# Kernel tuning notes

Hardware: AMD Instinct MI355X
Metric: run time of the kernel (lower is better)

Reference implementation:

```python
import jax, jax.numpy as jnp
import numpy as np

H, DH = 8, 64            # heads, dim_head (module defaults)
B, N, DN, DE = 1, 512, 128, 64  # batch, nodes, node feat, edge feat
INNER = H * DH


def _w(key, fan_in, fan_out):
    return jax.random.normal(key, (fan_in, fan_out), jnp.float32) / np.sqrt(fan_in)


def setup_inputs() -> dict:
    key = jax.random.key(0)
    ks = jax.random.split(key, 8)
    return {
        "nodes": jax.random.normal(ks[0], (B, N, DN), jnp.float32),
        "edges": jax.random.normal(ks[1], (B, N, N, DE), jnp.float32),
        "mask": jnp.ones((B, N), dtype=bool),
        "Wq": _w(ks[2], DN, INNER), "bq": jnp.zeros((INNER,), jnp.float32),
        "Wk": _w(ks[3], DN, INNER), "bk": jnp.zeros((INNER,), jnp.float32),
        "Wv": _w(ks[4], DN, INNER), "bv": jnp.zeros((INNER,), jnp.float32),
        "We": _w(ks[5], DE, INNER), "be": jnp.zeros((INNER,), jnp.float32),
        "Wo": _w(ks[6], INNER, DN), "bo": jnp.zeros((DN,), jnp.float32),
    }


def _split_heads(x):
    # (b, ..., h*d) -> (b*h, ..., d), matching rearrange 'b ... (h d) -> (b h) ... d'
    b = x.shape[0]
    mid = x.shape[1:-1]
    x = x.reshape(b, *mid, H, DH)
    x = jnp.moveaxis(x, -2, 1)              # (b, h, ..., d)
    return x.reshape(b * H, *mid, DH)


def reference(nodes, edges, mask, Wq, bq, Wk, bk, Wv, bv, We, be, Wo, bo):
    scale = DH ** (-0.5)
    q = _split_heads(nodes @ Wq + bq)        # (bh, n, d)
    k = _split_heads(nodes @ Wk + bk)        # (bh, n, d)
    v = _split_heads(nodes @ Wv + bv)        # (bh, n, d)
    e = _split_heads(edges @ We + be)        # (bh, n, n, d) -- ek == ev == e_kv
    k = k[:, None, :, :] + e                 # (bh, i, j, d) per-ij keys
    v = v[:, None, :, :] + e                 # (bh, i, j, d) per-ij values
    sim = jnp.einsum('bid,bijd->bij', q, k) * scale
    m = mask[:, :, None] & mask[:, None, :]  # (b, i, j)
    m = jnp.repeat(m, H, axis=0)             # (bh, i, j)
    sim = jnp.where(m, sim, -jnp.finfo(sim.dtype).max)
    attn = jax.nn.softmax(sim, axis=-1)
    out = jnp.einsum('bij,bijd->bid', attn, v)           # (bh, n, d)
    out = out.reshape(B, H, N, DH).transpose(0, 2, 1, 3).reshape(B, N, INNER)
    return out @ Wo + bo                                  # (b, n, d_node)
```

## Files before the change

### kernel.cpp

```cpp
#include <hip/hip_runtime.h>
#include <hip/hip_bf16.h>

#define NN 512
#define DNODE 128
#define DEDGE 64
#define NH 8
#define DHD 64
#define DIN 512
#define SCALE 0.125f

typedef unsigned short u16;
typedef unsigned int u32;

__device__ __forceinline__ float bf2f(u16 b) {
    u32 u = ((u32)b) << 16;
    return __builtin_bit_cast(float, u);
}
__device__ __forceinline__ u16 f2bf(float f) {
    u32 u = __builtin_bit_cast(u32, f);
    return (u16)((u + 0x7fffu + ((u >> 16) & 1u)) >> 16);
}
__device__ __forceinline__ float bflo(u32 u) { return __builtin_bit_cast(float, u << 16); }
__device__ __forceinline__ float bfhi(u32 u) { return __builtin_bit_cast(float, u & 0xffff0000u); }

__global__ __launch_bounds__(256) void k_qkv(
    const float* __restrict__ nodes,
    const float* __restrict__ Wq, const float* __restrict__ bq,
    const float* __restrict__ Wk, const float* __restrict__ bk,
    const float* __restrict__ Wv, const float* __restrict__ bv,
    float* __restrict__ Qo, float* __restrict__ Ko, float* __restrict__ Vo)
{
    const int it = blockIdx.x, ct = blockIdx.y, which = blockIdx.z;
    const float* W    = which == 0 ? Wq : (which == 1 ? Wk : Wv);
    const float* bias = which == 0 ? bq : (which == 1 ? bk : bv);
    float* O          = which == 0 ? Qo : (which == 1 ? Ko : Vo);
    __shared__ float As[64][132];
    __shared__ float Bs[128][68];
    const int t = threadIdx.x;
    const int ibase = it * 64, cbase = ct * 64;
#pragma unroll
    for (int p = 0; p < 8; ++p) {
        int r = p * 8 + (t >> 5), c4 = (t & 31) * 4;
        *(float4*)&As[r][c4] = *(const float4*)(nodes + (ibase + r) * DNODE + c4);
    }
#pragma unroll
    for (int p = 0; p < 8; ++p) {
        int k = p * 16 + (t >> 4), c4 = (t & 15) * 4;
        *(float4*)&Bs[k][c4] = *(const float4*)(W + k * DIN + cbase + c4);
    }
    __syncthreads();
    const int tx = t & 15, ty = t >> 4;
    float acc[4][4] = {};
    for (int k = 0; k < DNODE; ++k) {
        float4 b4 = *(const float4*)&Bs[k][tx * 4];
#pragma unroll
        for (int e = 0; e < 4; ++e) {
            float a = As[ty * 4 + e][k];
            acc[e][0] += a * b4.x; acc[e][1] += a * b4.y;
            acc[e][2] += a * b4.z; acc[e][3] += a * b4.w;
        }
    }
    const int h = ct;
#pragma unroll
    for (int ii = 0; ii < 4; ++ii) {
        int i = ibase + ty * 4 + ii;
        float4 o;
        o.x = acc[ii][0] + bias[cbase + tx * 4 + 0];
        o.y = acc[ii][1] + bias[cbase + tx * 4 + 1];
        o.z = acc[ii][2] + bias[cbase + tx * 4 + 2];
        o.w = acc[ii][3] + bias[cbase + tx * 4 + 3];
        *(float4*)(O + ((size_t)h * NN + i) * DHD + tx * 4) = o;
    }
}

__global__ __launch_bounds__(256) void k_qe(
    const float* __restrict__ Q, const float* __restrict__ We, float* __restrict__ QE)
{
    const int it = blockIdx.x, h = blockIdx.y;
    __shared__ float Qs[64][68];
    __shared__ float WsT[64][68];
    const int t = threadIdx.x;
    const int ibase = it * 64;
#pragma unroll
    for (int p = 0; p < 4; ++p) {
        int r = p * 16 + (t >> 4), d4 = (t & 15) * 4;
        *(float4*)&Qs[r][d4] = *(const float4*)(Q + ((size_t)h * NN + ibase + r) * DHD + d4);
    }
#pragma unroll
    for (int p = 0; p < 4; ++p) {
        int c = p * 16 + (t >> 4), d4 = (t & 15) * 4;
        float4 v = *(const float4*)(We + c * DIN + h * DHD + d4);
        WsT[d4 + 0][c] = v.x; WsT[d4 + 1][c] = v.y;
        WsT[d4 + 2][c] = v.z; WsT[d4 + 3][c] = v.w;
    }
    __syncthreads();
    const int tx = t & 15, ty = t >> 4;
    float acc[4][4] = {};
    for (int d = 0; d < DHD; ++d) {
        float4 b4 = *(const float4*)&WsT[d][tx * 4];
#pragma unroll
        for (int e = 0; e < 4; ++e) {
            float a = Qs[ty * 4 + e][d];
            acc[e][0] += a * b4.x; acc[e][1] += a * b4.y;
            acc[e][2] += a * b4.z; acc[e][3] += a * b4.w;
        }
    }
#pragma unroll
    for (int ii = 0; ii < 4; ++ii) {
        int i = ibase + ty * 4 + ii;
        float4 o;
        o.x = SCALE * acc[ii][0]; o.y = SCALE * acc[ii][1];
        o.z = SCALE * acc[ii][2]; o.w = SCALE * acc[ii][3];
        *(float4*)(QE + ((size_t)h * NN + i) * DEDGE + tx * 4) = o;
    }
}

__global__ __launch_bounds__(256) void k_qk(
    const float* __restrict__ Q, const float* __restrict__ K, float* __restrict__ QK)
{
    const int jt = blockIdx.x, it = blockIdx.y, h = blockIdx.z;
    __shared__ float Qs[64][68];
    __shared__ float KsT[64][68];
    const int t = threadIdx.x;
    const int ibase = it * 64, jbase = jt * 64;
#pragma unroll
    for (int p = 0; p < 4; ++p) {
        int r = p * 16 + (t >> 4), d4 = (t & 15) * 4;
        *(float4*)&Qs[r][d4] = *(const float4*)(Q + ((size_t)h * NN + ibase + r) * DHD + d4);
    }
#pragma unroll
    for (int p = 0; p < 4; ++p) {
        int j = p * 16 + (t >> 4), d4 = (t & 15) * 4;
        float4 v = *(const float4*)(K + ((size_t)h * NN + jbase + j) * DHD + d4);
        KsT[d4 + 0][j] = v.x; KsT[d4 + 1][j] = v.y;
        KsT[d4 + 2][j] = v.z; KsT[d4 + 3][j] = v.w;
    }
    __syncthreads();
    const int tx = t & 15, ty = t >> 4;
    float acc[4][4] = {};
    for (int d = 0; d < DHD; ++d) {
        float4 b4 = *(const float4*)&KsT[d][tx * 4];
#pragma unroll
        for (int e = 0; e < 4; ++e) {
            float a = Qs[ty * 4 + e][d];
            acc[e][0] += a * b4.x; acc[e][1] += a * b4.y;
            acc[e][2] += a * b4.z; acc[e][3] += a * b4.w;
        }
    }
#pragma unroll
    for (int ii = 0; ii < 4; ++ii) {
        int i = ibase + ty * 4 + ii;
        float4 o;
        o.x = SCALE * acc[ii][0]; o.y = SCALE * acc[ii][1];
        o.z = SCALE * acc[ii][2]; o.w = SCALE * acc[ii][3];
        *(float4*)(QK + ((size_t)h * NN + i) * NN + jbase + tx * 4) = o;
    }
}

__global__ __launch_bounds__(512, 4) void k_fused(
    const float* __restrict__ edges, const float* __restrict__ QK,
    const float* __restrict__ QE, float* __restrict__ AE, u16* __restrict__ P)
{
    __shared__ u16 erow[NN * 64];
    __shared__ u16 PlT[NH * 520];
    __shared__ float qes[NH][DEDGE];
    __shared__ float ae_acc[NH * 65];
    const int i = blockIdx.x;
    const int t = threadIdx.x;
    const int lane = t & 63, w = t >> 6;

    const float* E = edges + (size_t)i * NN * DEDGE;
    const int jst = t >> 3, c0 = (t & 7) * 8;
    float4 fa[8], fb[8];
#pragma unroll
    for (int p = 0; p < 8; ++p) {
        const float* s = E + (p * 64 + jst) * 64 + c0;
        fa[p] = *(const float4*)s;
        fb[p] = *(const float4*)(s + 4);
    }
    const float* qk = QK + ((size_t)w * NN + i) * NN;
    float qkr[8];
#pragma unroll
    for (int r = 0; r < 8; ++r) qkr[r] = qk[r * 64 + lane];
    qes[w][lane] = QE[((size_t)w * NN + i) * DEDGE + lane];
#pragma unroll
    for (int z = t; z < NH * 65; z += 512) ae_acc[z] = 0.f;

#pragma unroll
    for (int p = 0; p < 8; ++p) {
        int j = p * 64 + jst;
        uint4 pk;
        pk.x = (u32)f2bf(fa[p].x) | ((u32)f2bf(fa[p].y) << 16);
        pk.y = (u32)f2bf(fa[p].z) | ((u32)f2bf(fa[p].w) << 16);
        pk.z = (u32)f2bf(fb[p].x) | ((u32)f2bf(fb[p].y) << 16);
        pk.w = (u32)f2bf(fb[p].z) | ((u32)f2bf(fb[p].w) << 16);
        int sb = (j * 128 + c0 * 2) ^ ((j & 7) << 4);
        *(uint4*)((char*)erow + sb) = pk;
    }
    __syncthreads();

    float sim[8];
#pragma unroll
    for (int r = 0; r < 8; ++r) sim[r] = qkr[r];
#pragma unroll
    for (int cb = 0; cb < 8; ++cb) {
        float4 qA = *(const float4*)&qes[w][cb * 8];
        float4 qB = *(const float4*)&qes[w][cb * 8 + 4];
#pragma unroll
        for (int r = 0; r < 8; ++r) {
            int j = r * 64 + lane;
            uint4 ev = *(const uint4*)((const char*)erow +
                        ((j * 128 + cb * 16) ^ ((j & 7) << 4)));
            sim[r] += qA.x * bflo(ev.x) + qA.y * bfhi(ev.x)
                    + qA.z * bflo(ev.y) + qA.w * bfhi(ev.y)
                    + qB.x * bflo(ev.z) + qB.y * bfhi(ev.z)
                    + qB.z * bflo(ev.w) + qB.w * bfhi(ev.w);
        }
    }

    float m = sim[0];
#pragma unroll
    for (int r = 1; r < 8; ++r) m = fmaxf(m, sim[r]);
#pragma unroll
    for (int s = 32; s >= 1; s >>= 1) m = fmaxf(m, __shfl_xor(m, s, 64));
    float pr[8], l = 0.f;
#pragma unroll
    for (int r = 0; r < 8; ++r) { pr[r] = __expf(sim[r] - m); l += pr[r]; }
#pragma unroll
    for (int s = 32; s >= 1; s >>= 1) l += __shfl_xor(l, s, 64);
    float inv = 1.f / l;
    u16* Pg = P + ((size_t)w * NN + i) * NN;
#pragma unroll
    for (int r = 0; r < 8; ++r) {
        u16 pb = f2bf(pr[r] * inv);
        PlT[w * 520 + r * 64 + lane] = pb;
        Pg[r * 64 + lane] = pb;
    }
    __syncthreads();

    const int cp = lane & 31, jh = lane >> 5;
    const int jbase = w * 64 + jh * 32;
    float ae0[8] = {}, ae1[8] = {};
#pragma unroll
    for (int jb = 0; jb < 4; ++jb) {
        int j0 = jbase + jb * 8;
        float elo[8], ehi[8];
#pragma unroll
        for (int k = 0; k < 8; ++k) {
            int j = j0 + k;
            u32 ew = *(const u32*)((const char*)erow +
                      ((j * 128 + cp * 4) ^ ((j & 7) << 4)));
            elo[k] = bflo(ew); ehi[k] = bfhi(ew);
        }
#pragma unroll
        for (int h = 0; h < 8; ++h) {
            uint4 pv = *(const uint4*)&PlT[h * 520 + j0];
            float p0 = bflo(pv.x), p1 = bfhi(pv.x), p2 = bflo(pv.y), p3 = bfhi(pv.y);
            float p4 = bflo(pv.z), p5 = bfhi(pv.z), p6 = bflo(pv.w), p7 = bfhi(pv.w);
            ae0[h] += p0 * elo[0] + p1 * elo[1] + p2 * elo[2] + p3 * elo[3]
                    + p4 * elo[4] + p5 * elo[5] + p6 * elo[6] + p7 * elo[7];
            ae1[h] += p0 * ehi[0] + p1 * ehi[1] + p2 * ehi[2] + p3 * ehi[3]
                    + p4 * ehi[4] + p5 * ehi[5] + p6 * ehi[6] + p7 * ehi[7];
        }
    }
#pragma unroll
    for (int h = 0; h < 8; ++h) {
        ae0[h] += __shfl_xor(ae0[h], 32, 64);
        ae1[h] += __shfl_xor(ae1[h], 32, 64);
    }
    if (lane < 32) {
#pragma unroll
        for (int h = 0; h < 8; ++h) {
            atomicAdd(&ae_acc[h * 65 + 2 * cp],     ae0[h]);
            atomicAdd(&ae_acc[h * 65 + 2 * cp + 1], ae1[h]);
        }
    }
    __syncthreads();
    AE[(((size_t)(t >> 6)) * NN + i) * DEDGE + (t & 63)] = ae_acc[(t >> 6) * 65 + (t & 63)];
}

__global__ __launch_bounds__(256) void k_pv(
    const u16* __restrict__ P, const float* __restrict__ V, float* __restrict__ OUTV)
{
    const int ks = blockIdx.x, it = blockIdx.y, h = blockIdx.z;
    __shared__ u16 Ps[64][136];
    __shared__ float Vs[128][68];
    const int t = threadIdx.x;
    const int ibase = it * 64, kbase = ks * 128;
#pragma unroll
    for (int p = 0; p < 4; ++p) {
        int r = p * 16 + (t >> 4), j8 = (t & 15) * 8;
        *(uint4*)&Ps[r][j8] = *(const uint4*)(P + ((size_t)h * NN + ibase + r) * NN + kbase + j8);
    }
#pragma unroll
    for (int p = 0; p < 8; ++p) {
        int j = p * 16 + (t >> 4), d4 = (t & 15) * 4;
        *(float4*)&Vs[j][d4] = *(const float4*)(V + ((size_t)h * NN + kbase + j) * DHD + d4);
    }
    __syncthreads();
    const int tx = t & 15, ty = t >> 4;
    float acc[4][4] = {};
    for (int k = 0; k < 128; ++k) {
        float4 b4 = *(const float4*)&Vs[k][tx * 4];
#pragma unroll
        for (int e = 0; e < 4; ++e) {
            float a = bf2f(Ps[ty * 4 + e][k]);
            acc[e][0] += a * b4.x; acc[e][1] += a * b4.y;
            acc[e][2] += a * b4.z; acc[e][3] += a * b4.w;
        }
    }
#pragma unroll
    for (int ii = 0; ii < 4; ++ii)
#pragma unroll
        for (int jj = 0; jj < 4; ++jj)
            unsafeAtomicAdd(&OUTV[((size_t)h * NN + ibase + ty * 4 + ii) * DHD + tx * 4 + jj],
                            acc[ii][jj]);
}

__global__ __launch_bounds__(256) void k_inner(
    const float* __restrict__ AE, const float* __restrict__ We, const float* __restrict__ be,
    const float* __restrict__ OUTV, float* __restrict__ INNER)
{
    const int it = blockIdx.x, h = blockIdx.y;
    __shared__ float AEs[64][68];
    __shared__ float Ws[64][68];
    const int t = threadIdx.x;
    const int ibase = it * 64;
#pragma unroll
    for (int p = 0; p < 4; ++p) {
        int r = p * 16 + (t >> 4), c4 = (t & 15) * 4;
        *(float4*)&AEs[r][c4] = *(const float4*)(AE + ((size_t)h * NN + ibase + r) * DEDGE + c4);
    }
#pragma unroll
    for (int p = 0; p < 4; ++p) {
        int c = p * 16 + (t >> 4), d4 = (t & 15) * 4;
        *(float4*)&Ws[c][d4] = *(const float4*)(We + c * DIN + h * DHD + d4);
    }
    __syncthreads();
    const int tx = t & 15, ty = t >> 4;
    float acc[4][4] = {};
    for (int c = 0; c < DEDGE; ++c) {
        float4 b4 = *(const float4*)&Ws[c][tx * 4];
#pragma unroll
        for (int e = 0; e < 4; ++e) {
            float a = AEs[ty * 4 + e][c];
            acc[e][0] += a * b4.x; acc[e][1] += a * b4.y;
            acc[e][2] += a * b4.z; acc[e][3] += a * b4.w;
        }
    }
#pragma unroll
    for (int ii = 0; ii < 4; ++ii) {
        int i = ibase + ty * 4 + ii;
        float4 ov = *(const float4*)(OUTV + ((size_t)h * NN + i) * DHD + tx * 4);
        float4 o;
        o.x = acc[ii][0] + ov.x + be[h * DHD + tx * 4 + 0];
        o.y = acc[ii][1] + ov.y + be[h * DHD + tx * 4 + 1];
        o.z = acc[ii][2] + ov.z + be[h * DHD + tx * 4 + 2];
        o.w = acc[ii][3] + ov.w + be[h * DHD + tx * 4 + 3];
        *(float4*)(INNER + (size_t)i * DIN + h * DHD + tx * 4) = o;
    }
}

__global__ __launch_bounds__(256) void k_out(
    const float* __restrict__ INNER, const float* __restrict__ Wo, const float* __restrict__ bo,
    float* __restrict__ out)
{
    const int ks = blockIdx.x, it = blockIdx.y;
    __shared__ float Is[64][68];
    __shared__ float Wos[64][136];
    const int t = threadIdx.x;
    const int ibase = it * 64, kbase = ks * 64;
#pragma unroll
    for (int p = 0; p < 4; ++p) {
        int r = p * 16 + (t >> 4), c4 = (t & 15) * 4;
        *(float4*)&Is[r][c4] = *(const float4*)(INNER + (size_t)(ibase + r) * DIN + kbase + c4);
    }
#pragma unroll
    for (int p = 0; p < 8; ++p) {
        int k = p * 8 + (t >> 5), n4 = (t & 31) * 4;
        *(float4*)&Wos[k][n4] = *(const float4*)(Wo + (size_t)(kbase + k) * DNODE + n4);
    }
    __syncthreads();
    const int tx = t & 15, ty = t >> 4;
    float acc[4][8] = {};
    for (int k = 0; k < 64; ++k) {
        float4 b0 = *(const float4*)&Wos[k][tx * 8];
        float4 b1 = *(const float4*)&Wos[k][tx * 8 + 4];
#pragma unroll
        for (int e = 0; e < 4; ++e) {
            float a = Is[ty * 4 + e][k];
            acc[e][0] += a * b0.x; acc[e][1] += a * b0.y;
            acc[e][2] += a * b0.z; acc[e][3] += a * b0.w;
            acc[e][4] += a * b1.x; acc[e][5] += a * b1.y;
            acc[e][6] += a * b1.z; acc[e][7] += a * b1.w;
        }
    }
#pragma unroll
    for (int ii = 0; ii < 4; ++ii)
#pragma unroll
        for (int nn = 0; nn < 8; ++nn) {
            float v = acc[ii][nn] + (ks == 0 ? bo[tx * 8 + nn] : 0.f);
            unsafeAtomicAdd(&out[(size_t)(ibase + ty * 4 + ii) * DNODE + tx * 8 + nn], v);
        }
}

extern "C" void kernel_launch(void* const* d_in, const int* in_sizes, int n_in,
                              void* d_out, int out_size, void* d_ws, size_t ws_size,
                              hipStream_t stream) {
    (void)in_sizes; (void)n_in; (void)out_size; (void)ws_size;
    const float* nodes = (const float*)d_in[0];
    const float* edges = (const float*)d_in[1];
    const float* Wq = (const float*)d_in[3];  const float* bq = (const float*)d_in[4];
    const float* Wk = (const float*)d_in[5];  const float* bk = (const float*)d_in[6];
    const float* Wv = (const float*)d_in[7];  const float* bv = (const float*)d_in[8];
    const float* We = (const float*)d_in[9];  const float* be = (const float*)d_in[10];
    const float* Wo = (const float*)d_in[11]; const float* bo = (const float*)d_in[12];
    float* out = (float*)d_out;

    float* ws    = (float*)d_ws;
    float* Qb    = ws;
    float* Kb    = Qb    + NH * NN * DHD;
    float* Vb    = Kb    + NH * NN * DHD;
    float* QEb   = Vb    + NH * NN * DHD;
    float* AEb   = QEb   + NH * NN * DHD;
    float* OUTVb = AEb   + NH * NN * DHD;
    float* INb   = OUTVb + NH * NN * DHD;
    float* QKb   = INb   + (size_t)NN * DIN;
    u16*   Pb    = (u16*)(QKb + (size_t)NH * NN * NN);

    hipMemsetAsync(OUTVb, 0, (size_t)NH * NN * DHD * sizeof(float), stream);
    hipMemsetAsync(out, 0, (size_t)NN * DNODE * sizeof(float), stream);

    k_qkv<<<dim3(8, 8, 3), 256, 0, stream>>>(nodes, Wq, bq, Wk, bk, Wv, bv, Qb, Kb, Vb);
    k_qe<<<dim3(8, 8), 256, 0, stream>>>(Qb, We, QEb);
    k_qk<<<dim3(8, 8, 8), 256, 0, stream>>>(Qb, Kb, QKb);
    k_fused<<<dim3(512), 512, 0, stream>>>(edges, QKb, QEb, AEb, Pb);
    k_pv<<<dim3(4, 8, 8), 256, 0, stream>>>(Pb, Vb, OUTVb);
    k_inner<<<dim3(8, 8), 256, 0, stream>>>(AEb, We, be, OUTVb, INb);
    k_out<<<dim3(8, 8), 256, 0, stream>>>(INb, Wo, bo, out);
}
```

Measured before the change: 217.8 us.

## Compute edge-query similarity with bf16 MFMA and cross-wave softmax reduction

```diff
diff --git a/kernel.cpp b/kernel.cpp
--- a/kernel.cpp
+++ b/kernel.cpp
@@ -11,6 +11,8 @@
 
 typedef unsigned short u16;
 typedef unsigned int u32;
+typedef short bf16x8 __attribute__((ext_vector_type(8)));
+typedef float f32x4 __attribute__((ext_vector_type(4)));
 
 __device__ __forceinline__ float bf2f(u16 b) {
     u32 u = ((u32)b) << 16;
@@ -163,11 +165,15 @@
 {
     __shared__ u16 erow[NN * 64];
     __shared__ u16 PlT[NH * 520];
-    __shared__ float qes[NH][DEDGE];
     __shared__ float ae_acc[NH * 65];
+    __shared__ float wred0[16][9];
+    __shared__ float wred1[16][9];
     const int i = blockIdx.x;
     const int t = threadIdx.x;
     const int lane = t & 63, w = t >> 6;
+    const int jl = lane & 15, hq = lane >> 4;
+    const int h0 = hq * 4;
+    const int jw = w * 64;
 
     const float* E = edges + (size_t)i * NN * DEDGE;
     const int jst = t >> 3, c0 = (t & 7) * 8;
@@ -178,13 +184,28 @@
         fa[p] = *(const float4*)s;
         fb[p] = *(const float4*)(s + 4);
     }
-    const float* qk = QK + ((size_t)w * NN + i) * NN;
-    float qkr[8];
-#pragma unroll
-    for (int r = 0; r < 8; ++r) qkr[r] = qk[r * 64 + lane];
-    qes[w][lane] = QE[((size_t)w * NN + i) * DEDGE + lane];
-#pragma unroll
+    float qkv[16];
+#pragma unroll
+    for (int jt = 0; jt < 4; ++jt)
+#pragma unroll
+        for (int r = 0; r < 4; ++r)
+            qkv[jt * 4 + r] = (hq < 2)
+                ? QK[((size_t)(h0 + r) * NN + i) * NN + jw + jt * 16 + jl] : 0.f;
+    float4 qa0 = {0,0,0,0}, qa1 = qa0, qa2 = qa0, qa3 = qa0;
+    if (jl < 8) {
+        const float* qe = QE + ((size_t)jl * NN + i) * DEDGE + hq * 8;
+        qa0 = *(const float4*)(qe + 0);
+        qa1 = *(const float4*)(qe + 4);
+        qa2 = *(const float4*)(qe + 32);
+        qa3 = *(const float4*)(qe + 36);
+    }
     for (int z = t; z < NH * 65; z += 512) ae_acc[z] = 0.f;
+
+    bf16x8 af0, af1;
+    af0[0]=(short)f2bf(qa0.x); af0[1]=(short)f2bf(qa0.y); af0[2]=(short)f2bf(qa0.z); af0[3]=(short)f2bf(qa0.w);
+    af0[4]=(short)f2bf(qa1.x); af0[5]=(short)f2bf(qa1.y); af0[6]=(short)f2bf(qa1.z); af0[7]=(short)f2bf(qa1.w);
+    af1[0]=(short)f2bf(qa2.x); af1[1]=(short)f2bf(qa2.y); af1[2]=(short)f2bf(qa2.z); af1[3]=(short)f2bf(qa2.w);
+    af1[4]=(short)f2bf(qa3.x); af1[5]=(short)f2bf(qa3.y); af1[6]=(short)f2bf(qa3.z); af1[7]=(short)f2bf(qa3.w);
 
 #pragma unroll
     for (int p = 0; p < 8; ++p) {
@@ -199,42 +220,82 @@
     }
     __syncthreads();
 
-    float sim[8];
-#pragma unroll
-    for (int r = 0; r < 8; ++r) sim[r] = qkr[r];
-#pragma unroll
-    for (int cb = 0; cb < 8; ++cb) {
-        float4 qA = *(const float4*)&qes[w][cb * 8];
-        float4 qB = *(const float4*)&qes[w][cb * 8 + 4];
-#pragma unroll
-        for (int r = 0; r < 8; ++r) {
-            int j = r * 64 + lane;
-            uint4 ev = *(const uint4*)((const char*)erow +
-                        ((j * 128 + cb * 16) ^ ((j & 7) << 4)));
-            sim[r] += qA.x * bflo(ev.x) + qA.y * bfhi(ev.x)
-                    + qA.z * bflo(ev.y) + qA.w * bfhi(ev.y)
-                    + qB.x * bflo(ev.z) + qB.y * bfhi(ev.z)
-                    + qB.z * bflo(ev.w) + qB.w * bfhi(ev.w);
-        }
-    }
-
-    float m = sim[0];
-#pragma unroll
-    for (int r = 1; r < 8; ++r) m = fmaxf(m, sim[r]);
-#pragma unroll
-    for (int s = 32; s >= 1; s >>= 1) m = fmaxf(m, __shfl_xor(m, s, 64));
-    float pr[8], l = 0.f;
-#pragma unroll
-    for (int r = 0; r < 8; ++r) { pr[r] = __expf(sim[r] - m); l += pr[r]; }
-#pragma unroll
-    for (int s = 32; s >= 1; s >>= 1) l += __shfl_xor(l, s, 64);
-    float inv = 1.f / l;
-    u16* Pg = P + ((size_t)w * NN + i) * NN;
-#pragma unroll
-    for (int r = 0; r < 8; ++r) {
-        u16 pb = f2bf(pr[r] * inv);
-        PlT[w * 520 + r * 64 + lane] = pb;
-        Pg[r * 64 + lane] = pb;
+    f32x4 acc[4] = {f32x4{0,0,0,0}, f32x4{0,0,0,0}, f32x4{0,0,0,0}, f32x4{0,0,0,0}};
+    const char* eb = (const char*)erow;
+#pragma unroll
+    for (int jt = 0; jt < 4; ++jt) {
+        int j = jw + jt * 16 + jl;
+        int x = (j & 7) << 4;
+        uint4 e0 = *(const uint4*)(eb + ((j * 128 + hq * 16) ^ x));
+        uint4 e1 = *(const uint4*)(eb + ((j * 128 + 64 + hq * 16) ^ x));
+        f32x4 a = acc[jt];
+        a = __builtin_amdgcn_mfma_f32_16x16x32_bf16(af0, __builtin_bit_cast(bf16x8, e0), a, 0, 0, 0);
+        a = __builtin_amdgcn_mfma_f32_16x16x32_bf16(af1, __builtin_bit_cast(bf16x8, e1), a, 0, 0, 0);
+        acc[jt] = a;
+    }
+#pragma unroll
+    for (int jt = 0; jt < 4; ++jt)
+#pragma unroll
+        for (int r = 0; r < 4; ++r) acc[jt][r] += qkv[jt * 4 + r];
+
+    float lred[4];
+#pragma unroll
+    for (int r = 0; r < 4; ++r) {
+        float m0 = fmaxf(fmaxf(acc[0][r], acc[1][r]), fmaxf(acc[2][r], acc[3][r]));
+        m0 = fmaxf(m0, __shfl_xor(m0, 1));
+        m0 = fmaxf(m0, __shfl_xor(m0, 2));
+        m0 = fmaxf(m0, __shfl_xor(m0, 4));
+        m0 = fmaxf(m0, __shfl_xor(m0, 8));
+        lred[r] = m0;
+    }
+    if (jl == 0 && hq < 2) {
+#pragma unroll
+        for (int r = 0; r < 4; ++r) wred0[h0 + r][w] = lred[r];
+    }
+    __syncthreads();
+    float mm[4];
+#pragma unroll
+    for (int r = 0; r < 4; ++r) {
+        float m = wred0[h0 + r][0];
+#pragma unroll
+        for (int ww = 1; ww < 8; ++ww) m = fmaxf(m, wred0[h0 + r][ww]);
+        mm[r] = m;
+    }
+#pragma unroll
+    for (int r = 0; r < 4; ++r) {
+        float ls = 0.f;
+#pragma unroll
+        for (int jt = 0; jt < 4; ++jt) {
+            float e = __expf(acc[jt][r] - mm[r]);
+            acc[jt][r] = e; ls += e;
+        }
+        ls += __shfl_xor(ls, 1);
+        ls += __shfl_xor(ls, 2);
+        ls += __shfl_xor(ls, 4);
+        ls += __shfl_xor(ls, 8);
+        lred[r] = ls;
+    }
+    if (jl == 0 && hq < 2) {
+#pragma unroll
+        for (int r = 0; r < 4; ++r) wred1[h0 + r][w] = lred[r];
+    }
+    __syncthreads();
+    if (hq < 2) {
+#pragma unroll
+        for (int r = 0; r < 4; ++r) {
+            float s = wred1[h0 + r][0];
+#pragma unroll
+            for (int ww = 1; ww < 8; ++ww) s += wred1[h0 + r][ww];
+            float inv = 1.f / s;
+            int h = h0 + r;
+#pragma unroll
+            for (int jt = 0; jt < 4; ++jt) {
+                int j = jw + jt * 16 + jl;
+                u16 pb = f2bf(acc[jt][r] * inv);
+                PlT[h * 520 + j] = pb;
+                P[((size_t)h * NN + i) * NN + j] = pb;
+            }
+        }
     }
     __syncthreads();
 
```

Measured after the change: 214.2 us. About the same (-1.6%).
